# Kernel tuning notes

Hardware: AMD Instinct MI355X
Metric: run time of the kernel (lower is better)

The kernel has to match this reference:

```python
import jax, jax.numpy as jnp
import numpy as np


def _pdists(X):
    # Pairwise Euclidean distances (torch.cdist, p=2) via the Gram trick.
    sq = jnp.sum(X * X, axis=1)                      # (bs,)
    d2 = sq[:, None] + sq[None, :] - 2.0 * (X @ X.T)  # (bs, bs)
    d2 = jnp.maximum(d2, 0.0)
    # safe sqrt: exact forward, finite gradient at 0
    pos = d2 > 0
    return jnp.where(pos, jnp.sqrt(jnp.where(pos, d2, 1.0)), 0.0)


def setup_inputs() -> dict:
    key = jax.random.key(0)
    k1, k2, k3 = jax.random.split(key, 3)
    bs, d = 4096, 512
    n_classes, n_domains = 4, 3
    X = jax.random.normal(k1, (bs, d), dtype=jnp.float32)
    ds = jax.random.randint(k2, (bs,), 0, n_domains, dtype=jnp.int64 if jax.config.read('jax_enable_x64') else jnp.int32)
    y = jax.random.randint(k3, (bs,), 0, n_classes, dtype=jnp.int64 if jax.config.read('jax_enable_x64') else jnp.int32)
    return {"X": X, "ds": ds, "y": y, "n_classes": n_classes, "n_domains": n_domains}


def reference(X, ds, y, n_classes, n_domains):
    # Equivalent to JointCCSA.LSA / JointCCSA.LS with norm=True, assuming every
    # class and domain value appears in the batch (what torch.unique would find).
    dists = _pdists(X)                                # (bs, bs)

    d_lt = ds[:, None] < ds[None, :]                  # domain pair (d1 < d2) ordering
    same_y = y[:, None] == y[None, :]
    y_lt = y[:, None] < y[None, :]                    # class pair (c1 < c2) ordering

    # SA loss: 0.5 * sum over (i,j) with y_i==y_j, ds_i<ds_j
    sa_loss = 0.5 * jnp.sum(jnp.where(same_y & d_lt, dists, 0.0))
    n_sa = n_classes * (n_domains * (n_domains - 1) // 2)
    sa_loss = sa_loss / n_sa

    # S loss: hinge on margin=1, 0.5 * sum over (i,j) with y_i<y_j, ds_i<ds_j
    margin = 1.0
    h = jnp.maximum(0.0, margin - dists)
    s_loss = 0.5 * jnp.sum(jnp.where(y_lt & d_lt, h, 0.0))
    n_s = (n_classes * (n_classes - 1) // 2) * (n_domains * (n_domains - 1) // 2)
    s_loss = s_loss / n_s

    return sa_loss, s_loss
```

## Files before the change

### kernel.cpp

```cpp
#include <hip/hip_runtime.h>
#include <hip/hip_bf16.h>
#include <stdint.h>

#define NROW 4096
#define DIM  512
#define BM   128
#define BN   128
#define BK   64
#define NKT  (DIM / BK)

typedef __attribute__((ext_vector_type(8))) short  short8;
typedef __attribute__((ext_vector_type(4))) float  floatx4;

typedef const __attribute__((address_space(1))) void gvoid_t;
typedef __attribute__((address_space(3))) void       svoid_t;

__device__ __forceinline__ unsigned short f32_to_bf16_rne(float f) {
    unsigned u = __float_as_uint(f);
    u += 0x7FFFu + ((u >> 16) & 1u);
    return (unsigned short)(u >> 16);
}

__global__ __launch_bounds__(256) void prep_kernel(
    const float* __restrict__ X, unsigned short* __restrict__ Xpre,
    float* __restrict__ sq, float* __restrict__ out)
{
    const int wave = threadIdx.x >> 6;
    const int lane = threadIdx.x & 63;
    const int row  = blockIdx.x * 4 + wave;
    const float4* xr = (const float4*)(X + (size_t)row * DIM);
    float4 v0 = xr[2 * lane];
    float4 v1 = xr[2 * lane + 1];
    float s = v0.x*v0.x + v0.y*v0.y + v0.z*v0.z + v0.w*v0.w
            + v1.x*v1.x + v1.y*v1.y + v1.z*v1.z + v1.w*v1.w;
    uint4 pk;
    pk.x = f32_to_bf16_rne(v0.x) | ((unsigned)f32_to_bf16_rne(v0.y) << 16);
    pk.y = f32_to_bf16_rne(v0.z) | ((unsigned)f32_to_bf16_rne(v0.w) << 16);
    pk.z = f32_to_bf16_rne(v1.x) | ((unsigned)f32_to_bf16_rne(v1.y) << 16);
    pk.w = f32_to_bf16_rne(v1.z) | ((unsigned)f32_to_bf16_rne(v1.w) << 16);
    const int G   = row >> 3;
    const int l3r = row & 7;
    const int kt  = lane >> 3;
    const int p   = (lane & 7) ^ l3r;
    *(uint4*)(Xpre + (size_t)G * 4096 + kt * 512 + l3r * 64 + p * 8) = pk;
    #pragma unroll
    for (int off = 32; off; off >>= 1) s += __shfl_xor(s, off);
    if (lane == 0) sq[row] = s;
    if (blockIdx.x == 0 && threadIdx.x < 2) out[threadIdx.x] = 0.0f;
}

__global__ __launch_bounds__(512, 4) void ccsa_kernel(
    const unsigned short* __restrict__ Xpre, const float* __restrict__ sq,
    const int* __restrict__ ds, const int* __restrict__ y,
    const int* __restrict__ ncls, const int* __restrict__ ndom,
    float* __restrict__ out)
{
    __shared__ __align__(16) unsigned short As[2][BM * BK];
    __shared__ __align__(16) unsigned short Bs[2][BN * BK];
    __shared__ float red[16];

    const int t = blockIdx.x;
    int r = (int)((sqrtf(8.0f * (float)t + 1.0f) - 1.0f) * 0.5f);
    while ((r + 1) * (r + 2) / 2 <= t) ++r;
    while (r * (r + 1) / 2 > t) --r;
    const int bj_t = r;
    const int bi_t = t - r * (r + 1) / 2;
    const bool diag = (bi_t == bj_t);
    const int bm0 = bi_t * BM;
    const int bn0 = bj_t * BN;
    const int GA = bm0 >> 3;
    const int GB = bn0 >> 3;

    const int tid    = threadIdx.x;
    const int wave   = tid >> 6;
    const int lane   = tid & 63;
    const int warp_m = wave >> 2;
    const int warp_n = wave & 3;

    floatx4 acc[4][2];
    #pragma unroll
    for (int a = 0; a < 4; ++a)
        #pragma unroll
        for (int b = 0; b < 2; ++b)
            acc[a][b] = (floatx4){0.f, 0.f, 0.f, 0.f};

    const int m15  = lane & 15;
    const int quad = lane >> 4;
    const int row7 = lane & 7;

    #define STAGE(buf, kt)                                                    \
        do {                                                                  \
            _Pragma("unroll")                                                 \
            for (int is = 0; is < 2; ++is) {                                  \
                const int c = is * 8 + wave;                                  \
                __builtin_amdgcn_global_load_lds(                             \
                    (gvoid_t*)(Xpre + (size_t)(GA + c) * 4096 + (kt) * 512    \
                               + lane * 8),                                   \
                    (svoid_t*)(&As[buf][c * 512 + lane * 8]), 16, 0, 0);      \
                __builtin_amdgcn_global_load_lds(                             \
                    (gvoid_t*)(Xpre + (size_t)(GB + c) * 4096 + (kt) * 512    \
                               + lane * 8),                                   \
                    (svoid_t*)(&Bs[buf][c * 512 + lane * 8]), 16, 0, 0);      \
            }                                                                 \
        } while (0)

    STAGE(0, 0);
    for (int kt = 0; kt < NKT; ++kt) {
        const int cur = kt & 1;
        __syncthreads();
        if (kt + 1 < NKT) STAGE(cur ^ 1, kt + 1);

        #pragma unroll
        for (int kh = 0; kh < 2; ++kh) {
            short8 a[4], b[2];
            const int chunk = (kh * 4 + quad) ^ row7;
            #pragma unroll
            for (int tt = 0; tt < 4; ++tt) {
                const int rla = warp_m * 64 + tt * 16 + m15;
                a[tt] = *(const short8*)(&As[cur][rla * 64 + chunk * 8]);
            }
            #pragma unroll
            for (int tt = 0; tt < 2; ++tt) {
                const int rlb = warp_n * 32 + tt * 16 + m15;
                b[tt] = *(const short8*)(&Bs[cur][rlb * 64 + chunk * 8]);
            }
            #pragma unroll
            for (int tm = 0; tm < 4; ++tm)
                #pragma unroll
                for (int tn = 0; tn < 2; ++tn)
                    acc[tm][tn] = __builtin_amdgcn_mfma_f32_16x16x32_bf16(
                        a[tm], b[tn], acc[tm][tn], 0, 0, 0);
        }
    }
    #undef STAGE

    float sqj[2]; int yj[2], dsj[2];
    #pragma unroll
    for (int tn = 0; tn < 2; ++tn) {
        const int j = bn0 + warp_n * 32 + tn * 16 + m15;
        sqj[tn] = sq[j]; yj[tn] = y[j]; dsj[tn] = ds[j];
    }
    float sa = 0.f, ss = 0.f;
    if (diag) {
        #pragma unroll
        for (int tm = 0; tm < 4; ++tm) {
            #pragma unroll
            for (int rr = 0; rr < 4; ++rr) {
                const int i = bm0 + warp_m * 64 + tm * 16 + quad * 4 + rr;
                const float sqi = sq[i];
                const int   yi  = y[i];
                const int   dsi = ds[i];
                #pragma unroll
                for (int tn = 0; tn < 2; ++tn) {
                    if (dsi < dsj[tn]) {
                        const float d2   = sqi + sqj[tn] - 2.0f * acc[tm][tn][rr];
                        const float dist = sqrtf(fmaxf(d2, 0.f));
                        if (yi == yj[tn])     sa += dist;
                        else if (yi < yj[tn]) ss += fmaxf(0.f, 1.f - dist);
                    }
                }
            }
        }
    } else {
        #pragma unroll
        for (int tm = 0; tm < 4; ++tm) {
            #pragma unroll
            for (int rr = 0; rr < 4; ++rr) {
                const int i = bm0 + warp_m * 64 + tm * 16 + quad * 4 + rr;
                const float sqi = sq[i];
                const int   yi  = y[i];
                const int   dsi = ds[i];
                #pragma unroll
                for (int tn = 0; tn < 2; ++tn) {
                    if (dsi != dsj[tn]) {
                        const float d2   = sqi + sqj[tn] - 2.0f * acc[tm][tn][rr];
                        const float dist = sqrtf(fmaxf(d2, 0.f));
                        if (yi == yj[tn]) {
                            sa += dist;
                        } else {
                            const bool take = (dsi < dsj[tn]) ? (yi < yj[tn])
                                                              : (yj[tn] < yi);
                            if (take) ss += fmaxf(0.f, 1.f - dist);
                        }
                    }
                }
            }
        }
    }
    #pragma unroll
    for (int off = 32; off; off >>= 1) {
        sa += __shfl_xor(sa, off);
        ss += __shfl_xor(ss, off);
    }
    if (lane == 0) { red[wave] = sa; red[8 + wave] = ss; }
    __syncthreads();
    if (tid == 0) {
        float tsa = 0.f, tss = 0.f;
        #pragma unroll
        for (int w = 0; w < 8; ++w) { tsa += red[w]; tss += red[8 + w]; }
        const int nc = *ncls, nd = *ndom;
        const float n_sa = (float)(nc * (nd * (nd - 1) / 2));
        const float n_s  = (float)((nc * (nc - 1) / 2) * (nd * (nd - 1) / 2));
        atomicAdd(out + 0, tsa * 0.5f / n_sa);
        atomicAdd(out + 1, tss * 0.5f / n_s);
    }
}

extern "C" void kernel_launch(void* const* d_in, const int* in_sizes, int n_in,
                              void* d_out, int out_size, void* d_ws, size_t ws_size,
                              hipStream_t stream) {
    (void)in_sizes; (void)n_in; (void)out_size; (void)ws_size;
    const float* X  = (const float*)d_in[0];
    const int*   ds = (const int*)d_in[1];
    const int*   y  = (const int*)d_in[2];
    const int*   nc = (const int*)d_in[3];
    const int*   nd = (const int*)d_in[4];
    float* out = (float*)d_out;

    unsigned short* Xpre = (unsigned short*)d_ws;
    float* sq = (float*)((char*)d_ws + (size_t)NROW * DIM * 2);

    prep_kernel<<<NROW / 4, 256, 0, stream>>>(X, Xpre, sq, out);
    const int ntiles = NROW / BM;
    const int nblocks = ntiles * (ntiles + 1) / 2;
    ccsa_kernel<<<nblocks, 512, 0, stream>>>(Xpre, sq, ds, y, nc, nd, out);
}
```

Baseline: 98.90 us.

## Switch to 32x32x16 MFMA, pack per-row metadata, skip B load on diagonal tiles

Replaces the 16x16x32 bf16 MFMA tiling with 32x32x16 MFMAs, so each wave issues fewer, larger matrix ops with fewer LDS fragment reads per k-step. The prep kernel now packs the squared norm together with a combined y/ds code into a float2 per row, so the epilogue does one load per row instead of three. Diagonal tiles reuse the A tile in LDS as B and skip loading the B tile. The packed code assumes ds < 4, and the epilogue accumulator layout had to be rewritten for the 32x32 output mapping.

```diff
diff --git a/kernel.cpp b/kernel.cpp
--- a/kernel.cpp
+++ b/kernel.cpp
@@ -9,8 +9,8 @@
 #define BK   64
 #define NKT  (DIM / BK)
 
-typedef __attribute__((ext_vector_type(8))) short  short8;
-typedef __attribute__((ext_vector_type(4))) float  floatx4;
+typedef __attribute__((ext_vector_type(8)))  short short8;
+typedef __attribute__((ext_vector_type(16))) float floatx16;
 
 typedef const __attribute__((address_space(1))) void gvoid_t;
 typedef __attribute__((address_space(3))) void       svoid_t;
@@ -22,8 +22,9 @@
 }
 
 __global__ __launch_bounds__(256) void prep_kernel(
-    const float* __restrict__ X, unsigned short* __restrict__ Xpre,
-    float* __restrict__ sq, float* __restrict__ out)
+    const float* __restrict__ X, const int* __restrict__ ds,
+    const int* __restrict__ y, unsigned short* __restrict__ Xpre,
+    float2* __restrict__ meta, float* __restrict__ out)
 {
     const int wave = threadIdx.x >> 6;
     const int lane = threadIdx.x & 63;
@@ -45,18 +46,18 @@
     *(uint4*)(Xpre + (size_t)G * 4096 + kt * 512 + l3r * 64 + p * 8) = pk;
     #pragma unroll
     for (int off = 32; off; off >>= 1) s += __shfl_xor(s, off);
-    if (lane == 0) sq[row] = s;
+    if (lane == 0)
+        meta[row] = make_float2(s, __int_as_float(y[row] * 4 + ds[row]));
     if (blockIdx.x == 0 && threadIdx.x < 2) out[threadIdx.x] = 0.0f;
 }
 
 __global__ __launch_bounds__(512, 4) void ccsa_kernel(
-    const unsigned short* __restrict__ Xpre, const float* __restrict__ sq,
-    const int* __restrict__ ds, const int* __restrict__ y,
+    const unsigned short* __restrict__ Xpre, const float2* __restrict__ meta,
     const int* __restrict__ ncls, const int* __restrict__ ndom,
     float* __restrict__ out)
 {
-    __shared__ __align__(16) unsigned short As[2][BM * BK];
-    __shared__ __align__(16) unsigned short Bs[2][BN * BK];
+    __shared__ __align__(16) unsigned short As[2 * BM * BK];
+    __shared__ __align__(16) unsigned short Bs[2 * BN * BK];
     __shared__ float red[16];
 
     const int t = blockIdx.x;
@@ -76,17 +77,23 @@
     const int lane   = tid & 63;
     const int warp_m = wave >> 2;
     const int warp_n = wave & 3;
-
-    floatx4 acc[4][2];
-    #pragma unroll
-    for (int a = 0; a < 4; ++a)
-        #pragma unroll
-        for (int b = 0; b < 2; ++b)
-            acc[a][b] = (floatx4){0.f, 0.f, 0.f, 0.f};
-
-    const int m15  = lane & 15;
-    const int quad = lane >> 4;
-    const int row7 = lane & 7;
+    const int l31    = lane & 31;
+    const int l7     = lane & 7;
+    const int h      = lane >> 5;
+
+    const int jcol = bn0 + warp_n * 32 + l31;
+    const float2 mj = meta[jcol];
+    const float sqj = mj.x;
+    const int   ydj = __float_as_int(mj.y);
+    const int   dj  = ydj & 3, yj = ydj >> 2;
+
+    floatx16 acc[2];
+    #pragma unroll
+    for (int a = 0; a < 2; ++a)
+        #pragma unroll
+        for (int e = 0; e < 16; ++e) acc[a][e] = 0.f;
+
+    const unsigned short* Bbase = diag ? As : Bs;
 
     #define STAGE(buf, kt)                                                    \
         do {                                                                  \
@@ -96,13 +103,20 @@
                 __builtin_amdgcn_global_load_lds(                             \
                     (gvoid_t*)(Xpre + (size_t)(GA + c) * 4096 + (kt) * 512    \
                                + lane * 8),                                   \
-                    (svoid_t*)(&As[buf][c * 512 + lane * 8]), 16, 0, 0);      \
-                __builtin_amdgcn_global_load_lds(                             \
-                    (gvoid_t*)(Xpre + (size_t)(GB + c) * 4096 + (kt) * 512    \
-                               + lane * 8),                                   \
-                    (svoid_t*)(&Bs[buf][c * 512 + lane * 8]), 16, 0, 0);      \
+                    (svoid_t*)(&As[(buf) * 8192 + c * 512 + lane * 8]),       \
+                    16, 0, 0);                                                \
+                if (!diag)                                                    \
+                    __builtin_amdgcn_global_load_lds(                         \
+                        (gvoid_t*)(Xpre + (size_t)(GB + c) * 4096 + (kt) * 512\
+                                   + lane * 8),                               \
+                        (svoid_t*)(&Bs[(buf) * 8192 + c * 512 + lane * 8]),   \
+                        16, 0, 0);                                            \
             }                                                                 \
         } while (0)
+
+    const int rowA0 = (warp_m * 64 + l31) * 64;
+    const int rowA1 = (warp_m * 64 + 32 + l31) * 64;
+    const int rowB  = (warp_n * 32 + l31) * 64;
 
     STAGE(0, 0);
     for (int kt = 0; kt < NKT; ++kt) {
@@ -111,77 +125,52 @@
         if (kt + 1 < NKT) STAGE(cur ^ 1, kt + 1);
 
         #pragma unroll
-        for (int kh = 0; kh < 2; ++kh) {
-            short8 a[4], b[2];
-            const int chunk = (kh * 4 + quad) ^ row7;
+        for (int s = 0; s < 4; ++s) {
+            const int phys = ((2 * s + h) ^ l7) * 8;
+            const short8 av0 = *(const short8*)(&As[cur * 8192 + rowA0 + phys]);
+            const short8 av1 = *(const short8*)(&As[cur * 8192 + rowA1 + phys]);
+            const short8 bv  = *(const short8*)(&Bbase[cur * 8192 + rowB + phys]);
+            acc[0] = __builtin_amdgcn_mfma_f32_32x32x16_bf16(av0, bv, acc[0], 0, 0, 0);
+            acc[1] = __builtin_amdgcn_mfma_f32_32x32x16_bf16(av1, bv, acc[1], 0, 0, 0);
+        }
+    }
+    #undef STAGE
+
+    float sa = 0.f, ss = 0.f;
+    #pragma unroll
+    for (int tm = 0; tm < 2; ++tm) {
+        float2 mi[16];
+        #pragma unroll
+        for (int reg = 0; reg < 16; ++reg) {
+            const int i = bm0 + warp_m * 64 + tm * 32
+                        + (reg & 3) + 8 * (reg >> 2) + 4 * h;
+            mi[reg] = meta[i];
+        }
+        if (diag) {
             #pragma unroll
-            for (int tt = 0; tt < 4; ++tt) {
-                const int rla = warp_m * 64 + tt * 16 + m15;
-                a[tt] = *(const short8*)(&As[cur][rla * 64 + chunk * 8]);
-            }
-            #pragma unroll
-            for (int tt = 0; tt < 2; ++tt) {
-                const int rlb = warp_n * 32 + tt * 16 + m15;
-                b[tt] = *(const short8*)(&Bs[cur][rlb * 64 + chunk * 8]);
-            }
-            #pragma unroll
-            for (int tm = 0; tm < 4; ++tm)
-                #pragma unroll
-                for (int tn = 0; tn < 2; ++tn)
-                    acc[tm][tn] = __builtin_amdgcn_mfma_f32_16x16x32_bf16(
-                        a[tm], b[tn], acc[tm][tn], 0, 0, 0);
-        }
-    }
-    #undef STAGE
-
-    float sqj[2]; int yj[2], dsj[2];
-    #pragma unroll
-    for (int tn = 0; tn < 2; ++tn) {
-        const int j = bn0 + warp_n * 32 + tn * 16 + m15;
-        sqj[tn] = sq[j]; yj[tn] = y[j]; dsj[tn] = ds[j];
-    }
-    float sa = 0.f, ss = 0.f;
-    if (diag) {
-        #pragma unroll
-        for (int tm = 0; tm < 4; ++tm) {
-            #pragma unroll
-            for (int rr = 0; rr < 4; ++rr) {
-                const int i = bm0 + warp_m * 64 + tm * 16 + quad * 4 + rr;
-                const float sqi = sq[i];
-                const int   yi  = y[i];
-                const int   dsi = ds[i];
-                #pragma unroll
-                for (int tn = 0; tn < 2; ++tn) {
-                    if (dsi < dsj[tn]) {
-                        const float d2   = sqi + sqj[tn] - 2.0f * acc[tm][tn][rr];
-                        const float dist = sqrtf(fmaxf(d2, 0.f));
-                        if (yi == yj[tn])     sa += dist;
-                        else if (yi < yj[tn]) ss += fmaxf(0.f, 1.f - dist);
-                    }
+            for (int reg = 0; reg < 16; ++reg) {
+                const int ydi = __float_as_int(mi[reg].y);
+                const int di = ydi & 3, yi = ydi >> 2;
+                if (di < dj) {
+                    const float d2   = mi[reg].x + sqj - 2.0f * acc[tm][reg];
+                    const float dist = sqrtf(fmaxf(d2, 0.f));
+                    if (yi == yj)     sa += dist;
+                    else if (yi < yj) ss += fmaxf(0.f, 1.f - dist);
                 }
             }
-        }
-    } else {
-        #pragma unroll
-        for (int tm = 0; tm < 4; ++tm) {
+        } else {
             #pragma unroll
-            for (int rr = 0; rr < 4; ++rr) {
-                const int i = bm0 + warp_m * 64 + tm * 16 + quad * 4 + rr;
-                const float sqi = sq[i];
-                const int   yi  = y[i];
-                const int   dsi = ds[i];
-                #pragma unroll
-                for (int tn = 0; tn < 2; ++tn) {
-                    if (dsi != dsj[tn]) {
-                        const float d2   = sqi + sqj[tn] - 2.0f * acc[tm][tn][rr];
-                        const float dist = sqrtf(fmaxf(d2, 0.f));
-                        if (yi == yj[tn]) {
-                            sa += dist;
-                        } else {
-                            const bool take = (dsi < dsj[tn]) ? (yi < yj[tn])
-                                                              : (yj[tn] < yi);
-                            if (take) ss += fmaxf(0.f, 1.f - dist);
-                        }
+            for (int reg = 0; reg < 16; ++reg) {
+                const int ydi = __float_as_int(mi[reg].y);
+                const int di = ydi & 3, yi = ydi >> 2;
+                if (di != dj) {
+                    const float d2   = mi[reg].x + sqj - 2.0f * acc[tm][reg];
+                    const float dist = sqrtf(fmaxf(d2, 0.f));
+                    if (yi == yj) {
+                        sa += dist;
+                    } else {
+                        const bool take = (di < dj) ? (yi < yj) : (yj < yi);
+                        if (take) ss += fmaxf(0.f, 1.f - dist);
                     }
                 }
             }
@@ -218,10 +207,10 @@
     float* out = (float*)d_out;
 
     unsigned short* Xpre = (unsigned short*)d_ws;
-    float* sq = (float*)((char*)d_ws + (size_t)NROW * DIM * 2);
-
-    prep_kernel<<<NROW / 4, 256, 0, stream>>>(X, Xpre, sq, out);
+    float2* meta = (float2*)((char*)d_ws + (size_t)NROW * DIM * 2);
+
+    prep_kernel<<<NROW / 4, 256, 0, stream>>>(X, ds, y, Xpre, meta, out);
     const int ntiles = NROW / BM;
     const int nblocks = ntiles * (ntiles + 1) / 2;
-    ccsa_kernel<<<nblocks, 512, 0, stream>>>(Xpre, sq, ds, y, nc, nd, out);
-}
+    ccsa_kernel<<<nblocks, 512, 0, stream>>>(Xpre, meta, nc, nd, out);
+}
```

Measured after the change: 103.3 us. 4.4% more time.

## Halve K tile, reuse A tile on diagonal blocks, pack metadata, raise occupancy

Applied to the files above, without the earlier changes.

Cuts BK from 64 to 32 and re-lays out the bf16 pre-pack as k-slab-major with a 4-way XOR swizzle, so each stage is a single contiguous 16-byte load per thread. Diagonal tiles read B from the A buffer and skip the second load. sq, y and ds are packed into one float2 metadata array, and the column metadata is loaded before the main loop. Launch bounds rise to 6 blocks per CU to raise occupancy, at the cost of twice as many barrier-separated k iterations and fewer registers per thread.

```diff
diff --git a/kernel.cpp b/kernel.cpp
--- a/kernel.cpp
+++ b/kernel.cpp
@@ -6,7 +6,7 @@
 #define DIM  512
 #define BM   128
 #define BN   128
-#define BK   64
+#define BK   32
 #define NKT  (DIM / BK)
 
 typedef __attribute__((ext_vector_type(8))) short  short8;
@@ -22,8 +22,9 @@
 }
 
 __global__ __launch_bounds__(256) void prep_kernel(
-    const float* __restrict__ X, unsigned short* __restrict__ Xpre,
-    float* __restrict__ sq, float* __restrict__ out)
+    const float* __restrict__ X, const int* __restrict__ ds,
+    const int* __restrict__ y, unsigned short* __restrict__ Xpre,
+    float2* __restrict__ meta, float* __restrict__ out)
 {
     const int wave = threadIdx.x >> 6;
     const int lane = threadIdx.x & 63;
@@ -38,25 +39,26 @@
     pk.y = f32_to_bf16_rne(v0.z) | ((unsigned)f32_to_bf16_rne(v0.w) << 16);
     pk.z = f32_to_bf16_rne(v1.x) | ((unsigned)f32_to_bf16_rne(v1.y) << 16);
     pk.w = f32_to_bf16_rne(v1.z) | ((unsigned)f32_to_bf16_rne(v1.w) << 16);
-    const int G   = row >> 3;
-    const int l3r = row & 7;
-    const int kt  = lane >> 3;
-    const int p   = (lane & 7) ^ l3r;
-    *(uint4*)(Xpre + (size_t)G * 4096 + kt * 512 + l3r * 64 + p * 8) = pk;
+    const int G     = row >> 3;
+    const int l3r   = row & 7;
+    const int kt32  = lane >> 2;
+    const int chunk = lane & 3;
+    const int p     = chunk ^ (row & 3);
+    *(uint4*)(Xpre + ((size_t)kt32 * 512 + G) * 256 + l3r * 32 + p * 8) = pk;
     #pragma unroll
     for (int off = 32; off; off >>= 1) s += __shfl_xor(s, off);
-    if (lane == 0) sq[row] = s;
+    if (lane == 0)
+        meta[row] = make_float2(s, __int_as_float(y[row] * 4 + ds[row]));
     if (blockIdx.x == 0 && threadIdx.x < 2) out[threadIdx.x] = 0.0f;
 }
 
-__global__ __launch_bounds__(512, 4) void ccsa_kernel(
-    const unsigned short* __restrict__ Xpre, const float* __restrict__ sq,
-    const int* __restrict__ ds, const int* __restrict__ y,
+__global__ __launch_bounds__(512, 6) void ccsa_kernel(
+    const unsigned short* __restrict__ Xpre, const float2* __restrict__ meta,
     const int* __restrict__ ncls, const int* __restrict__ ndom,
     float* __restrict__ out)
 {
-    __shared__ __align__(16) unsigned short As[2][BM * BK];
-    __shared__ __align__(16) unsigned short Bs[2][BN * BK];
+    __shared__ __align__(16) unsigned short As[2 * BM * BK];
+    __shared__ __align__(16) unsigned short Bs[2 * BN * BK];
     __shared__ float red[16];
 
     const int t = blockIdx.x;
@@ -76,6 +78,18 @@
     const int lane   = tid & 63;
     const int warp_m = wave >> 2;
     const int warp_n = wave & 3;
+    const int m15    = lane & 15;
+    const int quad   = lane >> 4;
+    const int sw     = m15 & 3;
+
+    float sqj[2]; int yj[2], dj[2];
+    #pragma unroll
+    for (int tn = 0; tn < 2; ++tn) {
+        const float2 mj = meta[bn0 + warp_n * 32 + tn * 16 + m15];
+        sqj[tn] = mj.x;
+        const int ydj = __float_as_int(mj.y);
+        dj[tn] = ydj & 3; yj[tn] = ydj >> 2;
+    }
 
     floatx4 acc[4][2];
     #pragma unroll
@@ -84,25 +98,21 @@
         for (int b = 0; b < 2; ++b)
             acc[a][b] = (floatx4){0.f, 0.f, 0.f, 0.f};
 
-    const int m15  = lane & 15;
-    const int quad = lane >> 4;
-    const int row7 = lane & 7;
+    const unsigned short* Bbase = diag ? As : Bs;
 
     #define STAGE(buf, kt)                                                    \
         do {                                                                  \
-            _Pragma("unroll")                                                 \
-            for (int is = 0; is < 2; ++is) {                                  \
-                const int c = is * 8 + wave;                                  \
+            __builtin_amdgcn_global_load_lds(                                 \
+                (gvoid_t*)(Xpre + ((size_t)(kt) * 512 + GA) * 256 + tid * 8), \
+                (svoid_t*)(&As[(buf) * 4096 + tid * 8]), 16, 0, 0);           \
+            if (!diag)                                                        \
                 __builtin_amdgcn_global_load_lds(                             \
-                    (gvoid_t*)(Xpre + (size_t)(GA + c) * 4096 + (kt) * 512    \
-                               + lane * 8),                                   \
-                    (svoid_t*)(&As[buf][c * 512 + lane * 8]), 16, 0, 0);      \
-                __builtin_amdgcn_global_load_lds(                             \
-                    (gvoid_t*)(Xpre + (size_t)(GB + c) * 4096 + (kt) * 512    \
-                               + lane * 8),                                   \
-                    (svoid_t*)(&Bs[buf][c * 512 + lane * 8]), 16, 0, 0);      \
-            }                                                                 \
+                    (gvoid_t*)(Xpre + ((size_t)(kt) * 512 + GB) * 256         \
+                               + tid * 8),                                    \
+                    (svoid_t*)(&Bs[(buf) * 4096 + tid * 8]), 16, 0, 0);       \
         } while (0)
+
+    const int physA = (quad ^ sw) * 8;
 
     STAGE(0, 0);
     for (int kt = 0; kt < NKT; ++kt) {
@@ -110,76 +120,53 @@
         __syncthreads();
         if (kt + 1 < NKT) STAGE(cur ^ 1, kt + 1);
 
-        #pragma unroll
-        for (int kh = 0; kh < 2; ++kh) {
-            short8 a[4], b[2];
-            const int chunk = (kh * 4 + quad) ^ row7;
+        short8 a[4], b[2];
+        #pragma unroll
+        for (int tt = 0; tt < 4; ++tt) {
+            const int rla = warp_m * 64 + tt * 16 + m15;
+            a[tt] = *(const short8*)(&As[cur * 4096 + rla * 32 + physA]);
+        }
+        #pragma unroll
+        for (int tt = 0; tt < 2; ++tt) {
+            const int rlb = warp_n * 32 + tt * 16 + m15;
+            b[tt] = *(const short8*)(&Bbase[cur * 4096 + rlb * 32 + physA]);
+        }
+        #pragma unroll
+        for (int tm = 0; tm < 4; ++tm)
             #pragma unroll
-            for (int tt = 0; tt < 4; ++tt) {
-                const int rla = warp_m * 64 + tt * 16 + m15;
-                a[tt] = *(const short8*)(&As[cur][rla * 64 + chunk * 8]);
-            }
+            for (int tn = 0; tn < 2; ++tn)
+                acc[tm][tn] = __builtin_amdgcn_mfma_f32_16x16x32_bf16(
+                    a[tm], b[tn], acc[tm][tn], 0, 0, 0);
+    }
+    #undef STAGE
+
+    float sa = 0.f, ss = 0.f;
+    #pragma unroll
+    for (int tm = 0; tm < 4; ++tm) {
+        #pragma unroll
+        for (int rr = 0; rr < 4; ++rr) {
+            const int i = bm0 + warp_m * 64 + tm * 16 + quad * 4 + rr;
+            const float2 mi = meta[i];
+            const int ydi = __float_as_int(mi.y);
+            const int di = ydi & 3, yi = ydi >> 2;
             #pragma unroll
-            for (int tt = 0; tt < 2; ++tt) {
-                const int rlb = warp_n * 32 + tt * 16 + m15;
-                b[tt] = *(const short8*)(&Bs[cur][rlb * 64 + chunk * 8]);
-            }
-            #pragma unroll
-            for (int tm = 0; tm < 4; ++tm)
-                #pragma unroll
-                for (int tn = 0; tn < 2; ++tn)
-                    acc[tm][tn] = __builtin_amdgcn_mfma_f32_16x16x32_bf16(
-                        a[tm], b[tn], acc[tm][tn], 0, 0, 0);
-        }
-    }
-    #undef STAGE
-
-    float sqj[2]; int yj[2], dsj[2];
-    #pragma unroll
-    for (int tn = 0; tn < 2; ++tn) {
-        const int j = bn0 + warp_n * 32 + tn * 16 + m15;
-        sqj[tn] = sq[j]; yj[tn] = y[j]; dsj[tn] = ds[j];
-    }
-    float sa = 0.f, ss = 0.f;
-    if (diag) {
-        #pragma unroll
-        for (int tm = 0; tm < 4; ++tm) {
-            #pragma unroll
-            for (int rr = 0; rr < 4; ++rr) {
-                const int i = bm0 + warp_m * 64 + tm * 16 + quad * 4 + rr;
-                const float sqi = sq[i];
-                const int   yi  = y[i];
-                const int   dsi = ds[i];
-                #pragma unroll
-                for (int tn = 0; tn < 2; ++tn) {
-                    if (dsi < dsj[tn]) {
-                        const float d2   = sqi + sqj[tn] - 2.0f * acc[tm][tn][rr];
+            for (int tn = 0; tn < 2; ++tn) {
+                if (diag) {
+                    if (di < dj[tn]) {
+                        const float d2   = mi.x + sqj[tn] - 2.0f * acc[tm][tn][rr];
                         const float dist = sqrtf(fmaxf(d2, 0.f));
                         if (yi == yj[tn])     sa += dist;
                         else if (yi < yj[tn]) ss += fmaxf(0.f, 1.f - dist);
                     }
-                }
-            }
-        }
-    } else {
-        #pragma unroll
-        for (int tm = 0; tm < 4; ++tm) {
-            #pragma unroll
-            for (int rr = 0; rr < 4; ++rr) {
-                const int i = bm0 + warp_m * 64 + tm * 16 + quad * 4 + rr;
-                const float sqi = sq[i];
-                const int   yi  = y[i];
-                const int   dsi = ds[i];
-                #pragma unroll
-                for (int tn = 0; tn < 2; ++tn) {
-                    if (dsi != dsj[tn]) {
-                        const float d2   = sqi + sqj[tn] - 2.0f * acc[tm][tn][rr];
+                } else {
+                    if (di != dj[tn]) {
+                        const float d2   = mi.x + sqj[tn] - 2.0f * acc[tm][tn][rr];
                         const float dist = sqrtf(fmaxf(d2, 0.f));
                         if (yi == yj[tn]) {
                             sa += dist;
                         } else {
-                            const bool take = (dsi < dsj[tn]) ? (yi < yj[tn])
-                                                              : (yj[tn] < yi);
+                            const bool take = (di < dj[tn]) ? (yi < yj[tn])
+                                                            : (yj[tn] < yi);
                             if (take) ss += fmaxf(0.f, 1.f - dist);
                         }
                     }
@@ -218,10 +205,10 @@
     float* out = (float*)d_out;
 
     unsigned short* Xpre = (unsigned short*)d_ws;
-    float* sq = (float*)((char*)d_ws + (size_t)NROW * DIM * 2);
-
-    prep_kernel<<<NROW / 4, 256, 0, stream>>>(X, Xpre, sq, out);
+    float2* meta = (float2*)((char*)d_ws + (size_t)NROW * DIM * 2);
+
+    prep_kernel<<<NROW / 4, 256, 0, stream>>>(X, ds, y, Xpre, meta, out);
     const int ntiles = NROW / BM;
     const int nblocks = ntiles * (ntiles + 1) / 2;
-    ccsa_kernel<<<nblocks, 512, 0, stream>>>(Xpre, sq, ds, y, nc, nd, out);
-}
+    ccsa_kernel<<<nblocks, 512, 0, stream>>>(Xpre, meta, nc, nd, out);
+}
```

After: 100.4 us. About the same (+1.5%).
